# Performance work log

Hardware: AMD Instinct MI355X
Metric: run time of the kernel (lower is better)

Reference implementation:

```python
import jax, jax.numpy as jnp
import numpy as np

B, D, H = 64, 768, 512            # batch, bert hidden, classifier hidden_dim
G0, C0 = 8192, 8                  # level-0 meta labels, children per meta
G1, C1 = 65536, 11                # level-1 meta labels, children per meta (incl. pad)
L = 670091                        # num labels; pad id == L, table has L+1 rows
K1, K2 = 32, 64                   # candidates_topk


def setup_inputs() -> dict:
    key = jax.random.key(0)
    ks = jax.random.split(key, 14)
    rn = lambda k, shp, s=1.0: jax.random.normal(k, shp, jnp.float32) * s
    w = 0.02  # xavier-ish init scale
    inp = {
        'feat5':   rn(ks[0], (B, D)),
        'feat8':   rn(ks[1], (B, D)),
        'featcat': rn(ks[2], (B, 3 * D)),
        'W0': rn(ks[3], (D, H), w),     'b0': jnp.zeros((H,), jnp.float32),
        'W1': rn(ks[4], (D, H), w),     'b1': jnp.zeros((H,), jnp.float32),
        'W2': rn(ks[5], (3 * D, H), w), 'b2': jnp.zeros((H,), jnp.float32),
        'E0': rn(ks[6], (G0, H), w),
        'E1': rn(ks[7], (G1, H), w),
        # padding row (index L) is zero, per self.Cn[-1].weight[-1].data.fill_(0)
        'E2': rn(ks[8], (L + 1, H), w).at[-1].set(0.0),
        'g0': jax.random.randint(ks[9], (G0, C0), 0, G1, dtype=jnp.int32),
        'g1': jax.random.randint(ks[10], (G1, C1), 0, L + 1, dtype=jnp.int32),
    }
    return inp


def reference(feat5, feat8, featcat, W0, b0, W1, b1, W2, b2, E0, E1, E2, g0, g1):
    gelu = lambda x: jax.nn.gelu(x, approximate=False)  # torch nn.GELU default (erf)
    # Cn_hidden (dropout is identity at eval)
    h0 = gelu(feat5 @ W0 + b0)      # [B,H]
    h1 = gelu(feat8 @ W1 + b1)      # [B,H]
    h2 = gelu(featcat @ W2 + b2)    # [B,H]

    # ---- level 0: score all G0 meta-labels (dense bmm) ----
    logits0 = jnp.einsum('gh,bh->bg', E0, h0)            # [B,G0]
    p0 = jax.nn.sigmoid(logits0)
    prev0 = jax.lax.stop_gradient(p0)                    # prev_logits = scores.detach()

    # ---- level 1: topk routing + gather + bmm ----
    sc1, idx1 = jax.lax.top_k(prev0, K1)                 # [B,K1]; prev_cands is arange -> identity map
    cands1 = g0[idx1].reshape(B, K1 * C0)                # [B,K1*C0] level-1 meta ids
    gsc1 = jnp.repeat(sc1, C0, axis=1)                   # candidates_scores flattened
    logits1 = jnp.einsum('bch,bh->bc', E1[cands1], h1)   # [B,K1*C0]
    p1 = jax.nn.sigmoid(logits1)
    w1 = p1 * gsc1
    prev1 = jax.lax.stop_gradient(p1)

    # ---- level 2 (final): topk routing into padded label groups ----
    sc2, idx2 = jax.lax.top_k(prev1, K2)                 # [B,K2]
    meta2 = jnp.take_along_axis(cands1, idx2, axis=1)    # indices into g1
    cands2 = g1[meta2].reshape(B, K2 * C1)               # [B,K2*C1] label ids (L == pad)
    gsc2 = jnp.repeat(sc2, C1, axis=1)
    logits2 = jnp.einsum('bch,bh->bc', E2[cands2], h2)   # pad rows of E2 are 0 -> logit 0
    # torch: where(logits==0, -inf, logits).sigmoid() -> pad positions score 0
    p2 = jnp.where(logits2 == 0.0, jnp.float32(0.0), jax.nn.sigmoid(logits2))
    w2 = p2 * gsc2

    return (p0, p1, p2, w1, w2, cands1, cands2)
```

## Files before the change

### kernel.cpp

```cpp
#include <hip/hip_runtime.h>
#include <math.h>

#define BB 64
#define D0 768
#define D2 2304
#define HH 512
#define BBHH (BB*HH)
#define NG0 8192
#define NC0 8
#define NCH1 11
#define TK1 32
#define TK2 64
#define NC1 (TK1*NC0)
#define NC2 (TK2*NCH1)
#define SPA 2
#define SPB 2
#define SPC 6
#define NSL (SPA+SPB+SPC)

__device__ __forceinline__ float sigmoidf_(float x){ return 1.0f/(1.0f+expf(-x)); }
__device__ __forceinline__ float geluf_(float x){ return 0.5f*x*(1.0f+erff(x*0.70710678118654752f)); }
__device__ __forceinline__ unsigned long long maxu64_(unsigned long long a, unsigned long long b){ return a>b?a:b; }
__device__ __forceinline__ float dot8_(float4 ha, float4 hb, float4 a, float4 c){
  return ha.x*a.x+ha.y*a.y+ha.z*a.z+ha.w*a.w + hb.x*c.x+hb.y*c.y+hb.z*c.z+hb.w*c.w;
}

__device__ __forceinline__ unsigned long long bitonic256_desc(
    unsigned long long key, int tid, unsigned long long* sbuf)
{
  #pragma unroll
  for (int k = 2; k <= 256; k <<= 1) {
    #pragma unroll
    for (int j = k >> 1; j > 0; j >>= 1) {
      unsigned long long other;
      if (j >= 64) {
        __syncthreads();
        sbuf[tid] = key;
        __syncthreads();
        other = sbuf[tid ^ j];
      } else {
        other = __shfl_xor(key, j, 64);
      }
      bool keep_max = ((tid & j) == 0) == ((tid & k) == 0);
      key = keep_max ? (key > other ? key : other)
                     : (key < other ? key : other);
    }
  }
  return key;
}

__global__ __launch_bounds__(256) void gemm_h_kernel(
    const float* __restrict__ feat5, const float* __restrict__ feat8,
    const float* __restrict__ featcat,
    const float* __restrict__ W0, const float* __restrict__ W1,
    const float* __restrict__ W2, float* __restrict__ P)
{
  __shared__ __align__(16) float At[32][68];
  __shared__ __align__(16) float Bt[32][36];
  const int bid = blockIdx.x, tid = threadIdx.x;
  const float* X; const float* W; int Dm, split, jt, slice;
  if (bid < 32)      { X=feat5;   W=W0; Dm=D0; int l=bid;    split=l&1; jt=(l>>1)*32; slice=split; }
  else if (bid < 64) { X=feat8;   W=W1; Dm=D0; int l=bid-32; split=l&1; jt=(l>>1)*32; slice=SPA+split; }
  else               { X=featcat; W=W2; Dm=D2; int l=bid-64; split=l%6; jt=(l/6)*32;  slice=SPA+SPB+split; }
  float* Pb = P + (size_t)slice*BBHH;
  int k0 = split*384;
  int ti = tid >> 4, tj = tid & 15;
  float acc[4][2] = {};
  for (int ks = 0; ks < 384; ks += 32) {
    #pragma unroll
    for (int it = 0; it < 2; ++it) {
      int q = tid + it*256;
      int b = q & 63, kq = q >> 6;
      float4 v = *(const float4*)(X + (size_t)b*Dm + k0 + ks + kq*4);
      At[kq*4+0][b]=v.x; At[kq*4+1][b]=v.y; At[kq*4+2][b]=v.z; At[kq*4+3][b]=v.w;
    }
    {
      int j4 = tid & 7, kk = tid >> 3;
      float4 v = *(const float4*)(W + (size_t)(k0+ks+kk)*HH + jt + j4*4);
      *(float4*)&Bt[kk][j4*4] = v;
    }
    __syncthreads();
    #pragma unroll
    for (int k = 0; k < 32; ++k) {
      float4 a = *(const float4*)&At[k][ti*4];
      float2 b = *(const float2*)&Bt[k][tj*2];
      float av[4] = {a.x,a.y,a.z,a.w};
      float bv[2] = {b.x,b.y};
      #pragma unroll
      for (int r=0;r<4;++r)
        #pragma unroll
        for (int c=0;c<2;++c) acc[r][c] += av[r]*bv[c];
    }
    __syncthreads();
  }
  #pragma unroll
  for (int r=0;r<4;++r)
    #pragma unroll
    for (int c=0;c<2;++c)
      Pb[(size_t)(ti*4+r)*HH + jt + tj*2 + c] = acc[r][c];
}

__global__ __launch_bounds__(256,2) void level0_kernel(
    const float* __restrict__ P, const float* __restrict__ b0v,
    const float* __restrict__ E0, float* __restrict__ p0out)
{
  __shared__ __align__(16) float At[32][20];
  __shared__ __align__(16) float Bt[32][68];
  const int bid = blockIdx.x, tid = threadIdx.x;
  const int slot = bid >> 3;
  const int gt = (bid & 7) * 16 + (slot >> 2);
  const int btile = slot & 3;
  const int ti = tid >> 4, tj = tid & 15;
  float acc[4] = {};
  for (int ks = 0; ks < HH; ks += 32) {
    {
      int bb = tid & 15, kq = tid >> 4;
      float2 a = make_float2(0.f, 0.f);
      #pragma unroll
      for (int s=0;s<SPA;++s){
        float2 p = *(const float2*)(P + (size_t)s*BBHH
                        + (size_t)(btile*16+bb)*HH + ks + kq*2);
        a.x += p.x; a.y += p.y;
      }
      float2 bv = *(const float2*)(b0v + ks + kq*2);
      At[kq*2+0][bb] = geluf_(a.x + bv.x);
      At[kq*2+1][bb] = geluf_(a.y + bv.y);
    }
    #pragma unroll
    for (int it=0; it<2; ++it) {
      int q = tid + it*256; int g = q & 63, kq = q >> 6;
      float4 v = *(const float4*)(E0 + (size_t)(gt*64+g)*HH + ks + kq*4);
      Bt[kq*4+0][g]=v.x; Bt[kq*4+1][g]=v.y; Bt[kq*4+2][g]=v.z; Bt[kq*4+3][g]=v.w;
    }
    __syncthreads();
    #pragma unroll
    for (int k=0;k<32;++k) {
      float a = At[k][ti];
      float4 b = *(const float4*)&Bt[k][tj*4];
      acc[0] += a*b.x; acc[1] += a*b.y; acc[2] += a*b.z; acc[3] += a*b.w;
    }
    __syncthreads();
  }
  #pragma unroll
  for (int c=0;c<4;++c)
    p0out[(size_t)(btile*16 + ti)*NG0 + gt*64 + tj*4 + c] = sigmoidf_(acc[c]);
}

__global__ __launch_bounds__(256) void topk1_level1_kernel(
    const float* __restrict__ p0, const int* __restrict__ g0,
    const float* __restrict__ P, const float* __restrict__ b1v,
    const float* __restrict__ E1,
    int* __restrict__ cands1_i, float* __restrict__ o_c1,
    float* __restrict__ o_p1, float* __restrict__ o_w1)
{
  const int bid = blockIdx.x, tid = threadIdx.x;
  const int b = bid & 63, q = bid >> 6;
  const int lane = tid & 63, wid = tid >> 6;
  __shared__ float h1row[HH];
  __shared__ unsigned long long sbuf[256];
  __shared__ unsigned long long slist[256];
  __shared__ float s_sc[TK1];
  __shared__ int   s_idx[TK1];
  __shared__ int   scnt;
  {
    int j = tid*2;
    float ax=0.f, ay=0.f;
    #pragma unroll
    for (int s=0;s<SPB;++s){
      float2 v = *(const float2*)(P + (size_t)(SPA+s)*BBHH + (size_t)b*HH + j);
      ax += v.x; ay += v.y;
    }
    float2 bv = *(const float2*)(b1v + j);
    h1row[j]   = geluf_(ax + bv.x);
    h1row[j+1] = geluf_(ay + bv.y);
  }
  if (tid==0) scnt = 0;
  const float* row = p0 + (size_t)b*NG0;
  const float4* rp = (const float4*)(row + tid*32);
  unsigned long long m = 0ull;
  #pragma unroll
  for (int t=0;t<8;++t){
    float4 v = rp[t];
    unsigned i0 = (unsigned)(tid*32 + t*4);
    m = maxu64_(m, ((unsigned long long)__float_as_uint(v.x)<<32) | (unsigned long long)(0xFFFFFFFFu-(i0+0)));
    m = maxu64_(m, ((unsigned long long)__float_as_uint(v.y)<<32) | (unsigned long long)(0xFFFFFFFFu-(i0+1)));
    m = maxu64_(m, ((unsigned long long)__float_as_uint(v.z)<<32) | (unsigned long long)(0xFFFFFFFFu-(i0+2)));
    m = maxu64_(m, ((unsigned long long)__float_as_uint(v.w)<<32) | (unsigned long long)(0xFFFFFFFFu-(i0+3)));
  }
  __syncthreads();
  unsigned long long sk = bitonic256_desc(m, tid, sbuf);
  __syncthreads();
  sbuf[tid] = sk;
  __syncthreads();
  unsigned long long t32 = sbuf[31];
  __syncthreads();
  #pragma unroll
  for (int t=0;t<8;++t){
    float4 v = rp[t];
    unsigned i0 = (unsigned)(tid*32 + t*4);
    unsigned long long k0 = ((unsigned long long)__float_as_uint(v.x)<<32) | (unsigned long long)(0xFFFFFFFFu-(i0+0));
    unsigned long long k1 = ((unsigned long long)__float_as_uint(v.y)<<32) | (unsigned long long)(0xFFFFFFFFu-(i0+1));
    unsigned long long k2 = ((unsigned long long)__float_as_uint(v.z)<<32) | (unsigned long long)(0xFFFFFFFFu-(i0+2));
    unsigned long long k3 = ((unsigned long long)__float_as_uint(v.w)<<32) | (unsigned long long)(0xFFFFFFFFu-(i0+3));
    if (k0 >= t32) { int p = atomicAdd(&scnt,1); if (p<256) slist[p]=k0; }
    if (k1 >= t32) { int p = atomicAdd(&scnt,1); if (p<256) slist[p]=k1; }
    if (k2 >= t32) { int p = atomicAdd(&scnt,1); if (p<256) slist[p]=k2; }
    if (k3 >= t32) { int p = atomicAdd(&scnt,1); if (p<256) slist[p]=k3; }
  }
  __syncthreads();
  int cnt = scnt;
  unsigned long long key2 = (tid < cnt) ? slist[tid] : 0ull;
  key2 = bitonic256_desc(key2, tid, sbuf);
  __syncthreads();
  sbuf[tid] = key2;
  __syncthreads();
  if (tid < TK1) {
    unsigned long long w = sbuf[tid];
    s_idx[tid] = (int)(0xFFFFFFFFu - (unsigned)(w & 0xFFFFFFFFull));
    s_sc[tid]  = __uint_as_float((unsigned)(w>>32));
  }
  __syncthreads();
  if (q==0 && tid < NC1) {
    int k = tid >> 3, c = tid & 7;
    int cand = g0[(size_t)s_idx[k]*NC0 + c];
    cands1_i[(size_t)b*NC1+tid] = cand;
    o_c1[(size_t)b*NC1+tid] = (float)cand;
  }
  float4 ha = *(const float4*)&h1row[lane*8];
  float4 hb = *(const float4*)&h1row[lane*8+4];
  int cid[4][4];
  #pragma unroll
  for (int j=0;j<4;++j){
    int cbase = (q + 4*j)*16 + wid*4;
    #pragma unroll
    for (int u=0;u<4;++u)
      cid[j][u] = g0[(size_t)s_idx[(cbase+u)>>3]*NC0 + ((cbase+u)&7)];
  }
  float4 a0,c0,a1,c1,a2,c2,a3,c3;
  {
    const float4* p0e=(const float4*)(E1+(size_t)cid[0][0]*HH);
    const float4* p1e=(const float4*)(E1+(size_t)cid[0][1]*HH);
    const float4* p2e=(const float4*)(E1+(size_t)cid[0][2]*HH);
    const float4* p3e=(const float4*)(E1+(size_t)cid[0][3]*HH);
    a0=p0e[lane*2]; c0=p0e[lane*2+1]; a1=p1e[lane*2]; c1=p1e[lane*2+1];
    a2=p2e[lane*2]; c2=p2e[lane*2+1]; a3=p3e[lane*2]; c3=p3e[lane*2+1];
  }
  #pragma unroll
  for (int j=0;j<4;++j){
    float4 na0,nc0,na1,nc1,na2,nc2,na3,nc3;
    if (j<3){
      const float4* p0e=(const float4*)(E1+(size_t)cid[j+1][0]*HH);
      const float4* p1e=(const float4*)(E1+(size_t)cid[j+1][1]*HH);
      const float4* p2e=(const float4*)(E1+(size_t)cid[j+1][2]*HH);
      const float4* p3e=(const float4*)(E1+(size_t)cid[j+1][3]*HH);
      na0=p0e[lane*2]; nc0=p0e[lane*2+1]; na1=p1e[lane*2]; nc1=p1e[lane*2+1];
      na2=p2e[lane*2]; nc2=p2e[lane*2+1]; na3=p3e[lane*2]; nc3=p3e[lane*2+1];
    }
    int cbase = (q + 4*j)*16 + wid*4;
    float s0=dot8_(ha,hb,a0,c0), s1=dot8_(ha,hb,a1,c1);
    float s2=dot8_(ha,hb,a2,c2), s3=dot8_(ha,hb,a3,c3);
    #pragma unroll
    for (int off=1; off<64; off<<=1) {
      s0 += __shfl_xor(s0, off);
      s1 += __shfl_xor(s1, off);
      s2 += __shfl_xor(s2, off);
      s3 += __shfl_xor(s3, off);
    }
    if (lane==0) {
      float p;
      p = sigmoidf_(s0); o_p1[(size_t)b*NC1+cbase+0]=p; o_w1[(size_t)b*NC1+cbase+0]=p*s_sc[(cbase+0)>>3];
      p = sigmoidf_(s1); o_p1[(size_t)b*NC1+cbase+1]=p; o_w1[(size_t)b*NC1+cbase+1]=p*s_sc[(cbase+1)>>3];
      p = sigmoidf_(s2); o_p1[(size_t)b*NC1+cbase+2]=p; o_w1[(size_t)b*NC1+cbase+2]=p*s_sc[(cbase+2)>>3];
      p = sigmoidf_(s3); o_p1[(size_t)b*NC1+cbase+3]=p; o_w1[(size_t)b*NC1+cbase+3]=p*s_sc[(cbase+3)>>3];
    }
    if (j<3){ a0=na0;c0=nc0;a1=na1;c1=nc1;a2=na2;c2=nc2;a3=na3;c3=nc3; }
  }
}

__global__ __launch_bounds__(256,2) void topk2_level2_kernel(
    const float* __restrict__ p1, const int* __restrict__ cands1_i,
    const int* __restrict__ g1,
    const float* __restrict__ P, const float* __restrict__ b2v,
    const float* __restrict__ E2,
    float* __restrict__ o_c2, float* __restrict__ o_p2, float* __restrict__ o_w2)
{
  const int bid = blockIdx.x, tid = threadIdx.x;
  const int b = bid & 63, q = bid >> 6;
  const int lane = tid & 63, wid = tid >> 6;
  __shared__ float h2row[HH];
  __shared__ unsigned long long sbuf[256];
  __shared__ float s_sc[TK2];
  __shared__ int   s_idx[TK2];
  __shared__ int   c1row[NC1];
  {
    int j = tid*2;
    float ax=0.f, ay=0.f;
    #pragma unroll
    for (int s=0;s<SPC;++s){
      float2 v = *(const float2*)(P + (size_t)(SPA+SPB+s)*BBHH + (size_t)b*HH + j);
      ax += v.x; ay += v.y;
    }
    float2 bv = *(const float2*)(b2v + j);
    h2row[j]   = geluf_(ax + bv.x);
    h2row[j+1] = geluf_(ay + bv.y);
  }
  c1row[tid] = cands1_i[(size_t)b*NC1 + tid];
  float v = p1[(size_t)b*NC1 + tid];
  unsigned long long key = ((unsigned long long)__float_as_uint(v)<<32) |
                           (unsigned long long)(0xFFFFFFFFu - (unsigned)tid);
  __syncthreads();
  key = bitonic256_desc(key, tid, sbuf);
  __syncthreads();
  sbuf[tid] = key;
  __syncthreads();
  if (tid < TK2) {
    unsigned long long w = sbuf[tid];
    s_idx[tid] = (int)(0xFFFFFFFFu - (unsigned)(w & 0xFFFFFFFFull));
    s_sc[tid]  = __uint_as_float((unsigned)(w>>32));
  }
  __syncthreads();
  if (q==0) {
    for (int e=tid; e<NC2; e+=256) {
      int k = e/NCH1, c = e - k*NCH1;
      int meta = c1row[s_idx[k]];
      int cand = g1[(size_t)meta*NCH1 + c];
      o_c2[(size_t)b*NC2+e] = (float)cand;
    }
  }
  float4 ha = *(const float4*)&h2row[lane*8];
  float4 hb = *(const float4*)&h2row[lane*8+4];
  int cid0[11], cid1[11];
  #pragma unroll
  for (int j=0;j<11;++j){
    int cb = q*88 + j*8 + wid*2;
    int k0i = (cb+0)/NCH1, c0i = (cb+0) - k0i*NCH1;
    int k1i = (cb+1)/NCH1, c1i = (cb+1) - k1i*NCH1;
    cid0[j] = g1[(size_t)c1row[s_idx[k0i]]*NCH1 + c0i];
    cid1[j] = g1[(size_t)c1row[s_idx[k1i]]*NCH1 + c1i];
  }
  float4 a0,c0,a1,c1;
  {
    const float4* p0e=(const float4*)(E2+(size_t)cid0[0]*HH);
    const float4* p1e=(const float4*)(E2+(size_t)cid1[0]*HH);
    a0=p0e[lane*2]; c0=p0e[lane*2+1]; a1=p1e[lane*2]; c1=p1e[lane*2+1];
  }
  #pragma unroll
  for (int j=0;j<11;++j){
    float4 na0,nc0,na1,nc1;
    if (j<10){
      const float4* p0e=(const float4*)(E2+(size_t)cid0[j+1]*HH);
      const float4* p1e=(const float4*)(E2+(size_t)cid1[j+1]*HH);
      na0=p0e[lane*2]; nc0=p0e[lane*2+1]; na1=p1e[lane*2]; nc1=p1e[lane*2+1];
    }
    int cbase = q*88 + j*8 + wid*2;
    int k0i = (cbase+0)/NCH1;
    int k1i = (cbase+1)/NCH1;
    float s0 = dot8_(ha,hb,a0,c0);
    float s1 = dot8_(ha,hb,a1,c1);
    #pragma unroll
    for (int off=1; off<64; off<<=1) {
      s0 += __shfl_xor(s0, off);
      s1 += __shfl_xor(s1, off);
    }
    if (lane==0) {
      float p;
      p = (s0==0.0f)?0.0f:sigmoidf_(s0); o_p2[(size_t)b*NC2+cbase+0]=p; o_w2[(size_t)b*NC2+cbase+0]=p*s_sc[k0i];
      p = (s1==0.0f)?0.0f:sigmoidf_(s1); o_p2[(size_t)b*NC2+cbase+1]=p; o_w2[(size_t)b*NC2+cbase+1]=p*s_sc[k1i];
    }
    if (j<10){ a0=na0;c0=nc0;a1=na1;c1=nc1; }
  }
}

extern "C" void kernel_launch(void* const* d_in, const int* in_sizes, int n_in,
                              void* d_out, int out_size, void* d_ws, size_t ws_size,
                              hipStream_t stream) {
  const float* feat5   = (const float*)d_in[0];
  const float* feat8   = (const float*)d_in[1];
  const float* featcat = (const float*)d_in[2];
  const float* W0 = (const float*)d_in[3];
  const float* b0 = (const float*)d_in[4];
  const float* W1 = (const float*)d_in[5];
  const float* b1 = (const float*)d_in[6];
  const float* W2 = (const float*)d_in[7];
  const float* b2 = (const float*)d_in[8];
  const float* E0 = (const float*)d_in[9];
  const float* E1 = (const float*)d_in[10];
  const float* E2 = (const float*)d_in[11];
  const int*   g0 = (const int*)d_in[12];
  const int*   g1 = (const int*)d_in[13];

  float* out = (float*)d_out;
  float* ws  = (float*)d_ws;

  size_t off = 0;
  float* P = ws + off; off += (size_t)NSL*BBHH;
  int*   cands1_i = (int*)(ws + off); off += (size_t)BB*NC1;

  float* o_p0 = out;
  float* o_p1 = o_p0 + (size_t)BB*NG0;
  float* o_p2 = o_p1 + (size_t)BB*NC1;
  float* o_w1 = o_p2 + (size_t)BB*NC2;
  float* o_w2 = o_w1 + (size_t)BB*NC1;
  float* o_c1 = o_w2 + (size_t)BB*NC2;
  float* o_c2 = o_c1 + (size_t)BB*NC1;

  gemm_h_kernel<<<dim3(160), dim3(256), 0, stream>>>(feat5, feat8, featcat, W0, W1, W2, P);
  level0_kernel<<<dim3(512), dim3(256), 0, stream>>>(P, b0, E0, o_p0);
  topk1_level1_kernel<<<dim3(256), dim3(256), 0, stream>>>(o_p0, g0, P, b1, E1,
      cands1_i, o_c1, o_p1, o_w1);
  topk2_level2_kernel<<<dim3(512), dim3(256), 0, stream>>>(o_p1, cands1_i, g1, P, b2, E2,
      o_c2, o_p2, o_w2);
}
```

Measured before the change: 88.51 us.

## Prefetch E0 into cache during GEMM and double the gather-kernel grids

The hidden-layer GEMM kernel gets 96 extra blocks. They stream all of E0 through the cache and do a dummy reduction, so the level-0 kernel should find E0 warm in L2 or MALL. The level-1 and level-2 gather kernels each launch twice as many blocks, and each block handles half as many candidates. This raises concurrency for the latency-bound embedding gathers and adds occupancy hints. The cost is that every extra block recomputes h1/h2 and re-runs the top-k bitonic sort, and the prefetch blocks compete with the GEMM for bandwidth.

```diff
diff --git a/kernel.cpp b/kernel.cpp
--- a/kernel.cpp
+++ b/kernel.cpp
@@ -53,11 +53,23 @@
     const float* __restrict__ feat5, const float* __restrict__ feat8,
     const float* __restrict__ featcat,
     const float* __restrict__ W0, const float* __restrict__ W1,
-    const float* __restrict__ W2, float* __restrict__ P)
+    const float* __restrict__ W2, const float* __restrict__ E0,
+    float* __restrict__ P, float* __restrict__ dummy)
 {
   __shared__ __align__(16) float At[32][68];
   __shared__ __align__(16) float Bt[32][36];
   const int bid = blockIdx.x, tid = threadIdx.x;
+  if (bid >= 160) {
+    const float4* e4 = (const float4*)E0;
+    const int total = NG0*HH/4;
+    float acc = 0.f;
+    for (int i = (bid-160)*256 + tid; i < total; i += 96*256) {
+      float4 v = e4[i];
+      acc += v.x + v.y + v.z + v.w;
+    }
+    if (acc == 1.0e38f) dummy[bid] = acc;
+    return;
+  }
   const float* X; const float* W; int Dm, split, jt, slice;
   if (bid < 32)      { X=feat5;   W=W0; Dm=D0; int l=bid;    split=l&1; jt=(l>>1)*32; slice=split; }
   else if (bid < 64) { X=feat8;   W=W1; Dm=D0; int l=bid-32; split=l&1; jt=(l>>1)*32; slice=SPA+split; }
@@ -146,7 +158,7 @@
     p0out[(size_t)(btile*16 + ti)*NG0 + gt*64 + tj*4 + c] = sigmoidf_(acc[c]);
 }
 
-__global__ __launch_bounds__(256) void topk1_level1_kernel(
+__global__ __launch_bounds__(256,2) void topk1_level1_kernel(
     const float* __restrict__ p0, const int* __restrict__ g0,
     const float* __restrict__ P, const float* __restrict__ b1v,
     const float* __restrict__ E1,
@@ -228,10 +240,10 @@
   }
   float4 ha = *(const float4*)&h1row[lane*8];
   float4 hb = *(const float4*)&h1row[lane*8+4];
-  int cid[4][4];
-  #pragma unroll
-  for (int j=0;j<4;++j){
-    int cbase = (q + 4*j)*16 + wid*4;
+  int cid[2][4];
+  #pragma unroll
+  for (int j=0;j<2;++j){
+    int cbase = (q + 8*j)*16 + wid*4;
     #pragma unroll
     for (int u=0;u<4;++u)
       cid[j][u] = g0[(size_t)s_idx[(cbase+u)>>3]*NC0 + ((cbase+u)&7)];
@@ -246,17 +258,17 @@
     a2=p2e[lane*2]; c2=p2e[lane*2+1]; a3=p3e[lane*2]; c3=p3e[lane*2+1];
   }
   #pragma unroll
-  for (int j=0;j<4;++j){
+  for (int j=0;j<2;++j){
     float4 na0,nc0,na1,nc1,na2,nc2,na3,nc3;
-    if (j<3){
-      const float4* p0e=(const float4*)(E1+(size_t)cid[j+1][0]*HH);
-      const float4* p1e=(const float4*)(E1+(size_t)cid[j+1][1]*HH);
-      const float4* p2e=(const float4*)(E1+(size_t)cid[j+1][2]*HH);
-      const float4* p3e=(const float4*)(E1+(size_t)cid[j+1][3]*HH);
+    if (j<1){
+      const float4* p0e=(const float4*)(E1+(size_t)cid[1][0]*HH);
+      const float4* p1e=(const float4*)(E1+(size_t)cid[1][1]*HH);
+      const float4* p2e=(const float4*)(E1+(size_t)cid[1][2]*HH);
+      const float4* p3e=(const float4*)(E1+(size_t)cid[1][3]*HH);
       na0=p0e[lane*2]; nc0=p0e[lane*2+1]; na1=p1e[lane*2]; nc1=p1e[lane*2+1];
       na2=p2e[lane*2]; nc2=p2e[lane*2+1]; na3=p3e[lane*2]; nc3=p3e[lane*2+1];
     }
-    int cbase = (q + 4*j)*16 + wid*4;
+    int cbase = (q + 8*j)*16 + wid*4;
     float s0=dot8_(ha,hb,a0,c0), s1=dot8_(ha,hb,a1,c1);
     float s2=dot8_(ha,hb,a2,c2), s3=dot8_(ha,hb,a3,c3);
     #pragma unroll
@@ -273,11 +285,11 @@
       p = sigmoidf_(s2); o_p1[(size_t)b*NC1+cbase+2]=p; o_w1[(size_t)b*NC1+cbase+2]=p*s_sc[(cbase+2)>>3];
       p = sigmoidf_(s3); o_p1[(size_t)b*NC1+cbase+3]=p; o_w1[(size_t)b*NC1+cbase+3]=p*s_sc[(cbase+3)>>3];
     }
-    if (j<3){ a0=na0;c0=nc0;a1=na1;c1=nc1;a2=na2;c2=nc2;a3=na3;c3=nc3; }
-  }
-}
-
-__global__ __launch_bounds__(256,2) void topk2_level2_kernel(
+    if (j<1){ a0=na0;c0=nc0;a1=na1;c1=nc1;a2=na2;c2=nc2;a3=na3;c3=nc3; }
+  }
+}
+
+__global__ __launch_bounds__(256,4) void topk2_level2_kernel(
     const float* __restrict__ p1, const int* __restrict__ cands1_i,
     const int* __restrict__ g1,
     const float* __restrict__ P, const float* __restrict__ b2v,
@@ -329,45 +341,35 @@
   }
   float4 ha = *(const float4*)&h2row[lane*8];
   float4 hb = *(const float4*)&h2row[lane*8+4];
-  int cid0[11], cid1[11];
+  int cid[11];
   #pragma unroll
   for (int j=0;j<11;++j){
-    int cb = q*88 + j*8 + wid*2;
-    int k0i = (cb+0)/NCH1, c0i = (cb+0) - k0i*NCH1;
-    int k1i = (cb+1)/NCH1, c1i = (cb+1) - k1i*NCH1;
-    cid0[j] = g1[(size_t)c1row[s_idx[k0i]]*NCH1 + c0i];
-    cid1[j] = g1[(size_t)c1row[s_idx[k1i]]*NCH1 + c1i];
-  }
-  float4 a0,c0,a1,c1;
+    int cb = q*44 + j*4 + wid;
+    int ki = cb/NCH1, ci = cb - ki*NCH1;
+    cid[j] = g1[(size_t)c1row[s_idx[ki]]*NCH1 + ci];
+  }
+  float4 a0,c0;
   {
-    const float4* p0e=(const float4*)(E2+(size_t)cid0[0]*HH);
-    const float4* p1e=(const float4*)(E2+(size_t)cid1[0]*HH);
-    a0=p0e[lane*2]; c0=p0e[lane*2+1]; a1=p1e[lane*2]; c1=p1e[lane*2+1];
+    const float4* pe=(const float4*)(E2+(size_t)cid[0]*HH);
+    a0=pe[lane*2]; c0=pe[lane*2+1];
   }
   #pragma unroll
   for (int j=0;j<11;++j){
-    float4 na0,nc0,na1,nc1;
+    float4 na0,nc0;
     if (j<10){
-      const float4* p0e=(const float4*)(E2+(size_t)cid0[j+1]*HH);
-      const float4* p1e=(const float4*)(E2+(size_t)cid1[j+1]*HH);
-      na0=p0e[lane*2]; nc0=p0e[lane*2+1]; na1=p1e[lane*2]; nc1=p1e[lane*2+1];
-    }
-    int cbase = q*88 + j*8 + wid*2;
-    int k0i = (cbase+0)/NCH1;
-    int k1i = (cbase+1)/NCH1;
+      const float4* pe=(const float4*)(E2+(size_t)cid[j+1]*HH);
+      na0=pe[lane*2]; nc0=pe[lane*2+1];
+    }
+    int cb = q*44 + j*4 + wid;
+    int ki = cb/NCH1;
     float s0 = dot8_(ha,hb,a0,c0);
-    float s1 = dot8_(ha,hb,a1,c1);
-    #pragma unroll
-    for (int off=1; off<64; off<<=1) {
-      s0 += __shfl_xor(s0, off);
-      s1 += __shfl_xor(s1, off);
-    }
+    #pragma unroll
+    for (int off=1; off<64; off<<=1) s0 += __shfl_xor(s0, off);
     if (lane==0) {
-      float p;
-      p = (s0==0.0f)?0.0f:sigmoidf_(s0); o_p2[(size_t)b*NC2+cbase+0]=p; o_w2[(size_t)b*NC2+cbase+0]=p*s_sc[k0i];
-      p = (s1==0.0f)?0.0f:sigmoidf_(s1); o_p2[(size_t)b*NC2+cbase+1]=p; o_w2[(size_t)b*NC2+cbase+1]=p*s_sc[k1i];
-    }
-    if (j<10){ a0=na0;c0=nc0;a1=na1;c1=nc1; }
+      float p = (s0==0.0f)?0.0f:sigmoidf_(s0);
+      o_p2[(size_t)b*NC2+cb]=p; o_w2[(size_t)b*NC2+cb]=p*s_sc[ki];
+    }
+    if (j<10){ a0=na0;c0=nc0; }
   }
 }
 
@@ -395,6 +397,7 @@
   size_t off = 0;
   float* P = ws + off; off += (size_t)NSL*BBHH;
   int*   cands1_i = (int*)(ws + off); off += (size_t)BB*NC1;
+  float* dummy = ws + off; off += 256;
 
   float* o_p0 = out;
   float* o_p1 = o_p0 + (size_t)BB*NG0;
@@ -404,10 +407,10 @@
   float* o_c1 = o_w2 + (size_t)BB*NC2;
   float* o_c2 = o_c1 + (size_t)BB*NC1;
 
-  gemm_h_kernel<<<dim3(160), dim3(256), 0, stream>>>(feat5, feat8, featcat, W0, W1, W2, P);
+  gemm_h_kernel<<<dim3(256), dim3(256), 0, stream>>>(feat5, feat8, featcat, W0, W1, W2, E0, P, dummy);
   level0_kernel<<<dim3(512), dim3(256), 0, stream>>>(P, b0, E0, o_p0);
-  topk1_level1_kernel<<<dim3(256), dim3(256), 0, stream>>>(o_p0, g0, P, b1, E1,
+  topk1_level1_kernel<<<dim3(512), dim3(256), 0, stream>>>(o_p0, g0, P, b1, E1,
       cands1_i, o_c1, o_p1, o_w1);
-  topk2_level2_kernel<<<dim3(512), dim3(256), 0, stream>>>(o_p1, cands1_i, g1, P, b2, E2,
+  topk2_level2_kernel<<<dim3(1024), dim3(256), 0, stream>>>(o_p1, cands1_i, g1, P, b2, E2,
       o_c2, o_p2, o_w2);
 }
```

New measurement: 89.48 us. About the same (+1.1%).
